# Kernel optimization log

Measured on AMD Instinct MI355X. Metric: run time of the kernel, lower is better.

The kernel has to match this reference:

```python
import jax, jax.numpy as jnp
import numpy as np

OUTPUT_DIM = 1024
D_K = 1024  # Lt feature dim
D_Q = 1024  # rnn_ht feature dim
SCALE = 1.0 / np.sqrt(64.0)  # hardcoded 64**0.5 in original, NOT sqrt(output_dim)


def setup_inputs() -> dict:
    key = jax.random.key(0)
    k1, k2, k3, k4 = jax.random.split(key, 4)
    B, Sq, Sk = 8, 2048, 2048
    Lt = jax.random.normal(k1, (B, Sk, D_K), dtype=jnp.float32)
    rnn_ht = jax.random.normal(k2, (B, Sq, D_Q), dtype=jnp.float32)
    # 'uniform' keras initializer: U(-0.05, 0.05)
    kernel = jax.random.uniform(k3, (2, D_K, OUTPUT_DIM), dtype=jnp.float32, minval=-0.05, maxval=0.05)
    W = jax.random.uniform(k4, (D_Q, OUTPUT_DIM), dtype=jnp.float32, minval=-0.05, maxval=0.05)
    return {"Lt": Lt, "rnn_ht": rnn_ht, "kernel": kernel, "W": W}


def reference(Lt, rnn_ht, kernel, W):
    WQ = jnp.einsum('bsd,de->bse', rnn_ht, W)          # [B, Sq, E]
    WK = jnp.einsum('bsd,de->bse', Lt, kernel[0])      # [B, Sk, E]
    WV = jnp.einsum('bsd,de->bse', Lt, kernel[1])      # [B, Sk, E]
    QK = jnp.einsum('bqe,bke->bqk', WQ, WK) * SCALE    # [B, Sq, Sk]
    weights = jax.nn.softmax(QK, axis=-1)
    context_vector = jnp.einsum('bqk,bke->bqe', weights, WV)  # [B, Sq, E]
    return (context_vector, weights)
```

## Files before the change

### kernel.cpp

```cpp
#include <hip/hip_runtime.h>


typedef __bf16 bf16x8 __attribute__((ext_vector_type(8)));
typedef __bf16 bf16x4 __attribute__((ext_vector_type(4)));
typedef float  f32x4  __attribute__((ext_vector_type(4)));

__device__ __forceinline__ void gload_lds16(const void* g, void* l) {
  __builtin_amdgcn_global_load_lds(
      (__attribute__((address_space(1))) void*)(g),
      (__attribute__((address_space(3))) void*)(uintptr_t)(l),
      16, 0, 0);
}

__device__ __forceinline__ void ldfrag4(bf16x8 (&f)[4], const __bf16* reg_,
                                        int rbase, int fm, int gq) {
#pragma unroll
  for (int i = 0; i < 4; ++i) {
    const int r = rbase + i * 16 + fm;
    f[i] = *(const bf16x8*)(reg_ + r * 32 + ((gq ^ ((r >> 1) & 3)) << 3));
  }
}

__device__ __forceinline__ void stage16(const __bf16* src, __bf16* dst,
                                        size_t rowstride, int wave, int lane) {
#pragma unroll
  for (int i = 0; i < 2; ++i) {
    const int chunk = wave * 2 + i;
    const int row = chunk * 16 + (lane >> 2);
    const int gg = (lane & 3) ^ ((row >> 1) & 3);
    gload_lds16(src + (size_t)row * rowstride + (gg << 3), dst + chunk * 512);
  }
}

template <int MH>
__device__ __forceinline__ void mfma16(f32x4 (&acc)[8][4], const bf16x8 (&a)[4],
                                       const bf16x8 (&b)[4]) {
#pragma unroll
  for (int mi = 0; mi < 4; ++mi)
#pragma unroll
    for (int nj = 0; nj < 4; ++nj)
      acc[MH * 4 + mi][nj] = __builtin_amdgcn_mfma_f32_16x16x32_bf16(
          a[mi], b[nj], acc[MH * 4 + mi][nj], 0, 0, 0);
}

#define PHASE_MID()                       \
  __builtin_amdgcn_sched_barrier(0);      \
  __builtin_amdgcn_s_barrier();           \
  __builtin_amdgcn_s_setprio(1)

#define PHASE_END()                       \
  __builtin_amdgcn_s_setprio(0);          \
  __builtin_amdgcn_sched_barrier(0);      \
  __builtin_amdgcn_s_barrier()

template <bool OUTBF16>
__global__ __launch_bounds__(512, 2)
void gemm_nt(const __bf16* __restrict__ Ap, const __bf16* __restrict__ Bp,
             void* __restrict__ Cp, int N, int K,
             unsigned long long sAb, unsigned long long sBb,
             unsigned long long sCb, float scale) {
  __shared__ __bf16 lds[65536];

  const int tid  = threadIdx.x;
  const int wave = tid >> 6;
  const int lane = tid & 63;
  const int wm   = (wave >> 2) * 128;
  const int wn   = (wave & 3) * 64;
  const int fm   = lane & 15;
  const int gq   = lane >> 4;

  int bx, by, bz;
  {
    const int nx = gridDim.x, ny = gridDim.y;
    const int d = blockIdx.x + nx * (blockIdx.y + ny * blockIdx.z);
    if (gridDim.z == 8) {
      bz = d & 7;
      const int s = d >> 3;
      bx = s % nx; by = s / nx;
    } else {
      const int cpx = (nx * ny) >> 3;
      const int s = (d & 7) * cpx + (d >> 3);
      bx = s % nx; by = s / nx; bz = 0;
    }
  }
  const size_t m0 = (size_t)by * 256;
  const size_t n0 = (size_t)bx * 256;
  const __bf16* Aa = Ap + (size_t)bz * sAb + m0 * (size_t)K;
  const __bf16* Ba = Bp + (size_t)bz * sBb + n0 * (size_t)K;

  __bf16* const As_ = lds;
  __bf16* const Bs_ = lds + 32768;
#define AREG(p, h) (As_ + (p) * 16384 + (h) * 8192)
#define BREG(p, h) (Bs_ + (p) * 16384 + (h) * 8192)

  f32x4 acc[8][4] = {};
  bf16x8 a[4], b[4];

  stage16(Ba + 0,  BREG(0, 0), K, wave, lane);
  stage16(Aa + 0,  AREG(0, 0), K, wave, lane);
  stage16(Ba + 32, BREG(0, 1), K, wave, lane);
  stage16(Aa + 32, AREG(0, 1), K, wave, lane);
  asm volatile("s_waitcnt vmcnt(4)" ::: "memory");
  stage16(Ba + 64, BREG(1, 0), K, wave, lane);
  stage16(Aa + 64, AREG(1, 0), K, wave, lane);
  stage16(Ba + 96, BREG(1, 1), K, wave, lane);
  asm volatile("s_waitcnt vmcnt(6)" ::: "memory");
  __builtin_amdgcn_s_barrier();

  const int niter = K >> 7;
  for (int it = 0; it < niter; ++it) {
    const int kt = it << 7;
    const bool s2 = (kt + 128) < K;

    ldfrag4(a, AREG(0, 0), wm, fm, gq);
    ldfrag4(b, BREG(0, 0), wn, fm, gq);
    stage16(Aa + kt + 96, AREG(1, 1), K, wave, lane);
    PHASE_MID();
    mfma16<0>(acc, a, b);
    PHASE_END();

    ldfrag4(a, AREG(0, 0), wm + 64, fm, gq);
    if (s2) stage16(Ba + kt + 128, BREG(0, 0), K, wave, lane);
    PHASE_MID();
    mfma16<1>(acc, a, b);
    PHASE_END();

    ldfrag4(a, AREG(0, 1), wm, fm, gq);
    ldfrag4(b, BREG(0, 1), wn, fm, gq);
    if (s2) stage16(Aa + kt + 128, AREG(0, 0), K, wave, lane);
    PHASE_MID();
    mfma16<0>(acc, a, b);
    PHASE_END();

    ldfrag4(a, AREG(0, 1), wm + 64, fm, gq);
    if (s2) stage16(Ba + kt + 160, BREG(0, 1), K, wave, lane);
    PHASE_MID();
    mfma16<1>(acc, a, b);
    __builtin_amdgcn_s_setprio(0);
    __builtin_amdgcn_sched_barrier(0);
    if (s2) { asm volatile("s_waitcnt vmcnt(6)" ::: "memory"); }
    else    { asm volatile("s_waitcnt vmcnt(0)" ::: "memory"); }
    __builtin_amdgcn_s_barrier();

    ldfrag4(a, AREG(1, 0), wm, fm, gq);
    ldfrag4(b, BREG(1, 0), wn, fm, gq);
    if (s2) stage16(Aa + kt + 160, AREG(0, 1), K, wave, lane);
    PHASE_MID();
    mfma16<0>(acc, a, b);
    PHASE_END();

    ldfrag4(a, AREG(1, 0), wm + 64, fm, gq);
    if (s2) stage16(Ba + kt + 192, BREG(1, 0), K, wave, lane);
    PHASE_MID();
    mfma16<1>(acc, a, b);
    PHASE_END();

    ldfrag4(a, AREG(1, 1), wm, fm, gq);
    ldfrag4(b, BREG(1, 1), wn, fm, gq);
    if (s2) stage16(Aa + kt + 192, AREG(1, 0), K, wave, lane);
    PHASE_MID();
    mfma16<0>(acc, a, b);
    PHASE_END();

    ldfrag4(a, AREG(1, 1), wm + 64, fm, gq);
    if (s2) stage16(Ba + kt + 224, BREG(1, 1), K, wave, lane);
    PHASE_MID();
    mfma16<1>(acc, a, b);
    __builtin_amdgcn_s_setprio(0);
    __builtin_amdgcn_sched_barrier(0);
    if (s2) { asm volatile("s_waitcnt vmcnt(6)" ::: "memory"); }
    __builtin_amdgcn_s_barrier();
  }

  const int col   = lane & 15;
  const int rquad = (lane >> 4) * 4;
#pragma unroll
  for (int mi = 0; mi < 8; ++mi) {
#pragma unroll
    for (int r = 0; r < 4; ++r) {
      const size_t row = m0 + wm + mi * 16 + rquad + r;
#pragma unroll
      for (int nj = 0; nj < 4; ++nj) {
        const size_t cidx =
            (size_t)bz * sCb + row * (size_t)N + n0 + wn + nj * 16 + col;
        if constexpr (OUTBF16) {
          ((__bf16*)Cp)[cidx] = (__bf16)acc[mi][nj][r];
        } else {
          ((float*)Cp)[cidx] = acc[mi][nj][r] * scale;
        }
      }
    }
  }
#undef AREG
#undef BREG
}

__global__ __launch_bounds__(256)
void cvt_transpose(const float* __restrict__ s0, const float* __restrict__ s1,
                   const float* __restrict__ s2, __bf16* __restrict__ d0,
                   __bf16* __restrict__ d1, __bf16* __restrict__ d2) {
  const float* s = blockIdx.z == 0 ? s0 : (blockIdx.z == 1 ? s1 : s2);
  __bf16* d      = blockIdx.z == 0 ? d0 : (blockIdx.z == 1 ? d1 : d2);
  __shared__ float tile[32][33];
  const int x  = blockIdx.x * 32 + threadIdx.x;
  const int y0 = blockIdx.y * 32;
  for (int j = threadIdx.y; j < 32; j += 8)
    tile[j][threadIdx.x] = s[(size_t)(y0 + j) * 1024 + x];
  __syncthreads();
  const int x2 = y0 + threadIdx.x;
  const int y2 = blockIdx.x * 32;
  for (int j = threadIdx.y; j < 32; j += 8)
    d[(size_t)(y2 + j) * 1024 + x2] = (__bf16)tile[threadIdx.x][j];
}

__global__ __launch_bounds__(256)
void cvt_bf16(const float* __restrict__ s0, __bf16* __restrict__ d0,
              const float* __restrict__ s1, __bf16* __restrict__ d1) {
  const float* s = blockIdx.z ? s1 : s0;
  __bf16* d      = blockIdx.z ? d1 : d0;
  const size_t i = ((size_t)blockIdx.x * 256 + threadIdx.x) * 4;
  float4 f = *(const float4*)(s + i);
  bf16x4 h = {(__bf16)f.x, (__bf16)f.y, (__bf16)f.z, (__bf16)f.w};
  *(bf16x4*)(d + i) = h;
}

__global__ __launch_bounds__(256)
void softmax_rows(float* __restrict__ Wt, __bf16* __restrict__ Pb) {
  const int t = threadIdx.x;
  float* p = Wt + (size_t)blockIdx.x * 2048;
  float4 a = ((float4*)p)[t];
  float4 b = ((float4*)p)[t + 256];

  float m = fmaxf(fmaxf(fmaxf(a.x, a.y), fmaxf(a.z, a.w)),
                  fmaxf(fmaxf(b.x, b.y), fmaxf(b.z, b.w)));
#pragma unroll
  for (int off = 32; off > 0; off >>= 1) m = fmaxf(m, __shfl_xor(m, off));
  __shared__ float red[8];
  if ((t & 63) == 0) red[t >> 6] = m;
  __syncthreads();
  m = fmaxf(fmaxf(red[0], red[1]), fmaxf(red[2], red[3]));

  a.x = __expf(a.x - m); a.y = __expf(a.y - m);
  a.z = __expf(a.z - m); a.w = __expf(a.w - m);
  b.x = __expf(b.x - m); b.y = __expf(b.y - m);
  b.z = __expf(b.z - m); b.w = __expf(b.w - m);
  float s = a.x + a.y + a.z + a.w + b.x + b.y + b.z + b.w;
#pragma unroll
  for (int off = 32; off > 0; off >>= 1) s += __shfl_xor(s, off);
  if ((t & 63) == 0) red[4 + (t >> 6)] = s;
  __syncthreads();
  s = red[4] + red[5] + red[6] + red[7];

  const float inv = 1.0f / s;
  a.x *= inv; a.y *= inv; a.z *= inv; a.w *= inv;
  b.x *= inv; b.y *= inv; b.z *= inv; b.w *= inv;
  ((float4*)p)[t] = a;
  ((float4*)p)[t + 256] = b;

  __bf16* pb = Pb + (size_t)blockIdx.x * 2048;
  bf16x4 ha = {(__bf16)a.x, (__bf16)a.y, (__bf16)a.z, (__bf16)a.w};
  bf16x4 hb = {(__bf16)b.x, (__bf16)b.y, (__bf16)b.z, (__bf16)b.w};
  *(bf16x4*)(pb + (size_t)t * 4) = ha;
  *(bf16x4*)(pb + (size_t)(t + 256) * 4) = hb;
}

extern "C" void kernel_launch(void* const* d_in, const int* in_sizes, int n_in,
                              void* d_out, int out_size, void* d_ws,
                              size_t ws_size, hipStream_t stream) {
  const float* Lt  = (const float*)d_in[0];
  const float* rnn = (const float*)d_in[1];
  const float* ker = (const float*)d_in[2];
  const float* W   = (const float*)d_in[3];

  float* ctx = (float*)d_out;
  float* wts = ctx + (size_t)16777216;

  __bf16* ws   = (__bf16*)d_ws;
  __bf16* Wt   = ws;
  __bf16* k0t  = Wt + (1u << 20);
  __bf16* k1t  = k0t + (1u << 20);
  __bf16* WQ   = k1t + (1u << 20);
  __bf16* WK   = WQ + (16u << 20);
  __bf16* WVt  = WK + (16u << 20);
  __bf16* Ltb  = WVt + (16u << 20);
  __bf16* rnnb = Ltb + (16u << 20);
  __bf16* Pb = Ltb;

  cvt_transpose<<<dim3(32, 32, 3), dim3(32, 8), 0, stream>>>(
      W, ker, ker + (1u << 20), Wt, k0t, k1t);

  cvt_bf16<<<dim3(16384, 1, 2), 256, 0, stream>>>(Lt, Ltb, rnn, rnnb);

  gemm_nt<true><<<dim3(4, 64, 1), 512, 0, stream>>>(
      rnnb, Wt, WQ, 1024, 1024, 0ull, 0ull, 0ull, 1.0f);
  gemm_nt<true><<<dim3(4, 64, 1), 512, 0, stream>>>(
      Ltb, k0t, WK, 1024, 1024, 0ull, 0ull, 0ull, 1.0f);

  gemm_nt<true><<<dim3(8, 4, 8), 512, 0, stream>>>(
      k1t, Ltb, WVt, 2048, 1024, 0ull, 2048ull * 1024ull,
      1024ull * 2048ull, 1.0f);

  gemm_nt<false><<<dim3(8, 8, 8), 512, 0, stream>>>(
      WQ, WK, wts, 2048, 1024, 2048ull * 1024ull, 2048ull * 1024ull,
      2048ull * 2048ull, 0.125f);

  softmax_rows<<<16384, 256, 0, stream>>>(wts, Pb);

  gemm_nt<false><<<dim3(4, 8, 8), 512, 0, stream>>>(
      Pb, WVt, ctx, 1024, 2048, 2048ull * 2048ull, 1024ull * 2048ull,
      2048ull * 1024ull, 1.0f);
}
```

Before: 584.4 us.

## Merge projection GEMMs into one kernel and give each block multiple tiles

Replaces the separate WQ/WK/WV projection launches with a single kernel where each of 256 blocks computes three tiles sequentially, and makes the QK GEMM process two M-tiles per block sharing the same K tile. The GEMM body is factored into a device function reused by the new kernels, and block-to-tile mapping is done manually with batch-interleaved indexing. This aims to cut launch overhead and tail effects and to improve L2 reuse, at the cost of less parallelism per launch and possible imbalance.

After: 555.9 us. 1.05x faster.

```diff
diff --git a/kernel.cpp b/kernel.cpp
--- a/kernel.cpp
+++ b/kernel.cpp
@@ -54,40 +54,10 @@
   __builtin_amdgcn_s_barrier()
 
 template <bool OUTBF16>
-__global__ __launch_bounds__(512, 2)
-void gemm_nt(const __bf16* __restrict__ Ap, const __bf16* __restrict__ Bp,
-             void* __restrict__ Cp, int N, int K,
-             unsigned long long sAb, unsigned long long sBb,
-             unsigned long long sCb, float scale) {
-  __shared__ __bf16 lds[65536];
-
-  const int tid  = threadIdx.x;
-  const int wave = tid >> 6;
-  const int lane = tid & 63;
-  const int wm   = (wave >> 2) * 128;
-  const int wn   = (wave & 3) * 64;
-  const int fm   = lane & 15;
-  const int gq   = lane >> 4;
-
-  int bx, by, bz;
-  {
-    const int nx = gridDim.x, ny = gridDim.y;
-    const int d = blockIdx.x + nx * (blockIdx.y + ny * blockIdx.z);
-    if (gridDim.z == 8) {
-      bz = d & 7;
-      const int s = d >> 3;
-      bx = s % nx; by = s / nx;
-    } else {
-      const int cpx = (nx * ny) >> 3;
-      const int s = (d & 7) * cpx + (d >> 3);
-      bx = s % nx; by = s / nx; bz = 0;
-    }
-  }
-  const size_t m0 = (size_t)by * 256;
-  const size_t n0 = (size_t)bx * 256;
-  const __bf16* Aa = Ap + (size_t)bz * sAb + m0 * (size_t)K;
-  const __bf16* Ba = Bp + (size_t)bz * sBb + n0 * (size_t)K;
-
+__device__ __forceinline__ void tile_gemm(
+    const __bf16* __restrict__ Aa, const __bf16* __restrict__ Ba,
+    void* __restrict__ Cp, size_t cbase, int N, int K, float scale,
+    __bf16* lds, int wave, int lane, int wm, int wn, int fm, int gq) {
   __bf16* const As_ = lds;
   __bf16* const Bs_ = lds + 32768;
 #define AREG(p, h) (As_ + (p) * 16384 + (h) * 8192)
@@ -178,11 +148,10 @@
   for (int mi = 0; mi < 8; ++mi) {
 #pragma unroll
     for (int r = 0; r < 4; ++r) {
-      const size_t row = m0 + wm + mi * 16 + rquad + r;
+      const size_t roff = (size_t)(wm + mi * 16 + rquad + r) * (size_t)N;
 #pragma unroll
       for (int nj = 0; nj < 4; ++nj) {
-        const size_t cidx =
-            (size_t)bz * sCb + row * (size_t)N + n0 + wn + nj * 16 + col;
+        const size_t cidx = cbase + roff + wn + nj * 16 + col;
         if constexpr (OUTBF16) {
           ((__bf16*)Cp)[cidx] = (__bf16)acc[mi][nj][r];
         } else {
@@ -193,6 +162,78 @@
   }
 #undef AREG
 #undef BREG
+}
+
+__global__ __launch_bounds__(512, 2)
+void proj_all(const __bf16* __restrict__ rnnb, const __bf16* __restrict__ Ltb,
+              const __bf16* __restrict__ Wt, const __bf16* __restrict__ k0t,
+              const __bf16* __restrict__ k1t, __bf16* __restrict__ WQ,
+              __bf16* __restrict__ WK, __bf16* __restrict__ WVt) {
+  __shared__ __bf16 lds[65536];
+  const int tid = threadIdx.x, wave = tid >> 6, lane = tid & 63;
+  const int wm = (wave >> 2) * 128, wn = (wave & 3) * 64;
+  const int fm = lane & 15, gq = lane >> 4;
+  const int d = blockIdx.x, x = d & 7, s = d >> 3;
+
+  {
+    const int bx = s & 3, by = x * 8 + (s >> 2);
+    const size_t ao = (size_t)by * 256 * 1024;
+    const size_t bo = (size_t)bx * 256 * 1024;
+    const size_t cb = (size_t)by * 256 * 1024 + (size_t)bx * 256;
+    tile_gemm<true>(rnnb + ao, Wt + bo, WQ, cb, 1024, 1024, 1.0f,
+                    lds, wave, lane, wm, wn, fm, gq);
+    tile_gemm<true>(Ltb + ao, k0t + bo, WK, cb, 1024, 1024, 1.0f,
+                    lds, wave, lane, wm, wn, fm, gq);
+  }
+  {
+    const int by = s >> 3, bx = s & 7;
+    tile_gemm<true>(k1t + (size_t)by * 256 * 1024,
+                    Ltb + (size_t)x * 2048 * 1024 + (size_t)bx * 256 * 1024,
+                    WVt,
+                    (size_t)x * 1024 * 2048 + (size_t)by * 256 * 2048 +
+                        (size_t)bx * 256,
+                    2048, 1024, 1.0f, lds, wave, lane, wm, wn, fm, gq);
+  }
+}
+
+__global__ __launch_bounds__(512, 2)
+void qk2(const __bf16* __restrict__ WQ, const __bf16* __restrict__ WK,
+         float* __restrict__ wts) {
+  __shared__ __bf16 lds[65536];
+  const int tid = threadIdx.x, wave = tid >> 6, lane = tid & 63;
+  const int wm = (wave >> 2) * 128, wn = (wave & 3) * 64;
+  const int fm = lane & 15, gq = lane >> 4;
+  const int d = blockIdx.x, x = d & 7, s = d >> 3;
+  const int by = s >> 3, bx = s & 7;
+
+  const __bf16* Qb = WQ + (size_t)x * 2048 * 1024;
+  const __bf16* Kb = WK + (size_t)x * 2048 * 1024 + (size_t)bx * 256 * 1024;
+  const size_t cb0 = (size_t)x * 2048 * 2048 + (size_t)bx * 256;
+
+  tile_gemm<false>(Qb + (size_t)by * 256 * 1024, Kb, wts,
+                   cb0 + (size_t)by * 256 * 2048, 2048, 1024, 0.125f,
+                   lds, wave, lane, wm, wn, fm, gq);
+  tile_gemm<false>(Qb + (size_t)(by + 4) * 256 * 1024, Kb, wts,
+                   cb0 + (size_t)(by + 4) * 256 * 2048, 2048, 1024, 0.125f,
+                   lds, wave, lane, wm, wn, fm, gq);
+}
+
+__global__ __launch_bounds__(512, 2)
+void pv1(const __bf16* __restrict__ Pb, const __bf16* __restrict__ WVt,
+         float* __restrict__ ctx) {
+  __shared__ __bf16 lds[65536];
+  const int tid = threadIdx.x, wave = tid >> 6, lane = tid & 63;
+  const int wm = (wave >> 2) * 128, wn = (wave & 3) * 64;
+  const int fm = lane & 15, gq = lane >> 4;
+  const int d = blockIdx.x, x = d & 7, s = d >> 3;
+  const int by = s >> 2, bx = s & 3;
+
+  tile_gemm<false>(Pb + (size_t)x * 2048 * 2048 + (size_t)by * 256 * 2048,
+                   WVt + (size_t)x * 1024 * 2048 + (size_t)bx * 256 * 2048,
+                   ctx,
+                   (size_t)x * 2048 * 1024 + (size_t)by * 256 * 1024 +
+                       (size_t)bx * 256,
+                   1024, 2048, 1.0f, lds, wave, lane, wm, wn, fm, gq);
 }
 
 __global__ __launch_bounds__(256)
@@ -291,22 +332,11 @@
 
   cvt_bf16<<<dim3(16384, 1, 2), 256, 0, stream>>>(Lt, Ltb, rnn, rnnb);
 
-  gemm_nt<true><<<dim3(4, 64, 1), 512, 0, stream>>>(
-      rnnb, Wt, WQ, 1024, 1024, 0ull, 0ull, 0ull, 1.0f);
-  gemm_nt<true><<<dim3(4, 64, 1), 512, 0, stream>>>(
-      Ltb, k0t, WK, 1024, 1024, 0ull, 0ull, 0ull, 1.0f);
-
-  gemm_nt<true><<<dim3(8, 4, 8), 512, 0, stream>>>(
-      k1t, Ltb, WVt, 2048, 1024, 0ull, 2048ull * 1024ull,
-      1024ull * 2048ull, 1.0f);
-
-  gemm_nt<false><<<dim3(8, 8, 8), 512, 0, stream>>>(
-      WQ, WK, wts, 2048, 1024, 2048ull * 1024ull, 2048ull * 1024ull,
-      2048ull * 2048ull, 0.125f);
+  proj_all<<<256, 512, 0, stream>>>(rnnb, Ltb, Wt, k0t, k1t, WQ, WK, WVt);
+
+  qk2<<<256, 512, 0, stream>>>(WQ, WK, wts);
 
   softmax_rows<<<16384, 256, 0, stream>>>(wts, Pb);
 
-  gemm_nt<false><<<dim3(4, 8, 8), 512, 0, stream>>>(
-      Pb, WVt, ctx, 1024, 2048, 2048ull * 2048ull, 1024ull * 2048ull,
-      2048ull * 1024ull, 1.0f);
-}
+  pv1<<<256, 512, 0, stream>>>(Pb, WVt, ctx);
+}
```
